# Performance work log

Measured on AMD Instinct MI355X. Metric: run time of the kernel, lower is better.

## Reference

```python
import jax, jax.numpy as jnp
import numpy as np

DIM = 512
NUM_HEADS = 4
SCALE = 1.0 / np.sqrt(DIM)  # note: module scales by 1/sqrt(dim), not 1/sqrt(head_dim)


def setup_inputs() -> dict:
    key = jax.random.key(0)
    k1, k2, k3, k4, k5, k6 = jax.random.split(key, 6)
    B, N, M, C = 8, 2048, 2048, DIM
    bound = 1.0 / np.sqrt(C)
    return {
        "F1": jax.random.normal(k1, (B, N, C), dtype=jnp.float32),
        "F2": jax.random.normal(k2, (B, M, C), dtype=jnp.float32),
        "W_qkv": jax.random.uniform(k3, (C, C), jnp.float32, -bound, bound),
        "b_qkv": jax.random.uniform(k4, (C,), jnp.float32, -bound, bound),
        "W_proj": jax.random.uniform(k5, (C, C), jnp.float32, -bound, bound),
        "b_proj": jax.random.uniform(k6, (C,), jnp.float32, -bound, bound),
    }


def reference(F1, F2, W_qkv, b_qkv, W_proj, b_proj):
    B, N, C = F1.shape
    M = F2.shape[1]
    H, D = NUM_HEADS, C // NUM_HEADS
    # shared qkv projection (same weights for q, k and v in the original module)
    q = (F1 @ W_qkv + b_qkv).reshape(B, N, H, D)  # queries from F1
    kv = (F2 @ W_qkv + b_qkv).reshape(B, M, H, D)  # keys == values from F2
    attn = jnp.einsum("bnhd,bmhd->bhnm", q * SCALE, kv)
    attn = jax.nn.softmax(attn, axis=-1)
    x = jnp.einsum("bhnm,bmhd->bnhd", attn, kv).reshape(B, N, C)
    return x @ W_proj + b_proj
```

## Files before the change

kernel.cpp:

```cpp
#include <hip/hip_runtime.h>
#include <math.h>


typedef __attribute__((ext_vector_type(8))) short s16x8;
typedef __attribute__((ext_vector_type(4))) float f32x4;

#define C_DIM 512
#define HDIM  128
#define NROWS 16384
#define SCALE_Q 0.04419417382415922f
#define LOG2E   1.4426950408889634f

__device__ __forceinline__ unsigned short f2bf(float f) {
    union { float f; unsigned u; } v; v.f = f;
    unsigned r = v.u + 0x7fffu + ((v.u >> 16) & 1u);
    return (unsigned short)(r >> 16);
}

__device__ __forceinline__ void async16(const void* g, void* l) {
    __builtin_amdgcn_global_load_lds(
        (const __attribute__((address_space(1))) void*)g,
        (__attribute__((address_space(3))) void*)l, 16, 0, 0);
}

__global__ __launch_bounds__(256)
void conv_bf16_2(const float* __restrict__ s0, const float* __restrict__ s1,
                 unsigned short* __restrict__ d0, unsigned short* __restrict__ d1,
                 int n8) {
    const float* src = blockIdx.y ? s1 : s0;
    unsigned short* dst = blockIdx.y ? d1 : d0;
    int i = blockIdx.x * 256 + threadIdx.x;
    if (i >= n8) return;
    float4 a = ((const float4*)src)[2 * i];
    float4 b = ((const float4*)src)[2 * i + 1];
    union { unsigned short us[8]; uint4 v; } o;
    o.us[0] = f2bf(a.x); o.us[1] = f2bf(a.y); o.us[2] = f2bf(a.z); o.us[3] = f2bf(a.w);
    o.us[4] = f2bf(b.x); o.us[5] = f2bf(b.y); o.us[6] = f2bf(b.z); o.us[7] = f2bf(b.w);
    ((uint4*)dst)[i] = o.v;
}

__global__ __launch_bounds__(256)
void wconv_t2(const float* __restrict__ W0, const float* __restrict__ W1,
              unsigned short* __restrict__ T0, unsigned short* __restrict__ T1) {
    const float* W = blockIdx.z ? W1 : W0;
    unsigned short* Wt = blockIdx.z ? T1 : T0;
    __shared__ float t[64][65];
    const int k0 = blockIdx.y * 64, n0 = blockIdx.x * 64;
    const int c = threadIdx.x & 63, r0 = threadIdx.x >> 6;
#pragma unroll
    for (int r = r0; r < 64; r += 4)
        t[r][c] = W[(size_t)(k0 + r) * C_DIM + n0 + c];
    __syncthreads();
#pragma unroll
    for (int r = r0; r < 64; r += 4)
        Wt[(size_t)(n0 + r) * C_DIM + k0 + c] = f2bf(t[c][r]);
}

__global__ __launch_bounds__(256)
void kv_transpose(const unsigned short* __restrict__ KV,
                  unsigned short* __restrict__ KVT) {
    __shared__ unsigned short t[64][66];
    const int key0 = blockIdx.x * 64;
    const int d0   = blockIdx.y * 64;
    const int bh   = blockIdx.z;
    const int b    = bh >> 2, h = bh & 3;
    const int c = threadIdx.x & 63, r0 = threadIdx.x >> 6;
    const unsigned short* src = KV + ((size_t)(b * 2048 + key0)) * C_DIM + h * HDIM + d0;
#pragma unroll
    for (int r = r0; r < 64; r += 4)
        t[r][c] = src[(size_t)r * C_DIM + c];
    __syncthreads();
    unsigned short* dst = KVT + ((size_t)(bh * HDIM + d0)) * 2048 + key0;
#pragma unroll
    for (int r = r0; r < 64; r += 4)
        dst[(size_t)r * 2048 + c] = t[c][r];
}

template <int OUT_BF16>
__global__ __launch_bounds__(256, 3)
void gemm_bt(const unsigned short* __restrict__ A,
             const unsigned short* __restrict__ Bt,
             const float* __restrict__ bias,
             void* __restrict__ Cv, float oscTop, int topRows) {
    __shared__ __align__(16) unsigned short As[128][64];
    __shared__ __align__(16) unsigned short Bs[128][64];

    const int tid  = threadIdx.x;
    const int wid  = tid >> 6;
    const int lane = tid & 63;
    const int lr   = lane & 15;
    const int quad = lane >> 4;
    const int wm   = wid >> 1;
    const int wn   = wid & 1;
    const int rowBase = blockIdx.y * 128;
    const int colBase = blockIdx.x * 128;
    const int srow = lane >> 3;
    const int soff = srow * C_DIM + (((lane & 7) ^ (srow & 7)) * 8);
    const float osc = (rowBase < topRows) ? oscTop : 1.0f;

    f32x4 acc[4][4];
#pragma unroll
    for (int i = 0; i < 4; i++)
#pragma unroll
        for (int j = 0; j < 4; j++) acc[i][j] = (f32x4)0.0f;

    for (int kt = 0; kt < 8; kt++) {
        const int k0 = kt * 64;
        __syncthreads();
#pragma unroll
        for (int i = 0; i < 4; i++) {
            const int R = wid * 32 + i * 8;
            async16(A  + (size_t)(rowBase + R) * C_DIM + k0 + soff, &As[R][0]);
            async16(Bt + (size_t)(colBase + R) * C_DIM + k0 + soff, &Bs[R][0]);
        }
        __syncthreads();

#pragma unroll
        for (int s = 0; s < 2; s++) {
            s16x8 af[4], bf[4];
#pragma unroll
            for (int i = 0; i < 4; i++)
                af[i] = *(const s16x8*)&As[wm * 64 + i * 16 + lr][((s * 4 + quad) ^ (lr & 7)) * 8];
#pragma unroll
            for (int j = 0; j < 4; j++)
                bf[j] = *(const s16x8*)&Bs[wn * 64 + j * 16 + lr][((s * 4 + quad) ^ (lr & 7)) * 8];
#pragma unroll
            for (int i = 0; i < 4; i++)
#pragma unroll
                for (int j = 0; j < 4; j++)
                    acc[i][j] = __builtin_amdgcn_mfma_f32_16x16x32_bf16(af[i], bf[j], acc[i][j], 0, 0, 0);
        }
    }

    float bcol[4];
#pragma unroll
    for (int j = 0; j < 4; j++)
        bcol[j] = bias[colBase + wn * 64 + j * 16 + lr];
#pragma unroll
    for (int i = 0; i < 4; i++) {
#pragma unroll
        for (int j = 0; j < 4; j++) {
            const int col = colBase + wn * 64 + j * 16 + lr;
#pragma unroll
            for (int r = 0; r < 4; r++) {
                const int row = rowBase + wm * 64 + i * 16 + quad * 4 + r;
                float v = (acc[i][j][r] + bcol[j]) * osc;
                if (OUT_BF16)
                    ((unsigned short*)Cv)[(size_t)row * C_DIM + col] = f2bf(v);
                else
                    ((float*)Cv)[(size_t)row * C_DIM + col] = v;
            }
        }
    }
}

__global__ __launch_bounds__(256, 2)
void cross_attn(const unsigned short* __restrict__ Q,
                const unsigned short* __restrict__ KV,
                const unsigned short* __restrict__ KVT,
                unsigned short* __restrict__ X) {
    __shared__ __align__(16) unsigned short Kt[2][64][128];
    __shared__ __align__(16) unsigned short Vt[2][128][64];
    __shared__ __align__(16) unsigned short Pl[4][32][64];

    const int tid  = threadIdx.x;
    const int wid  = tid >> 6;
    const int lane = tid & 63;
    const int lr   = lane & 15;
    const int quad = lane >> 4;

    const int wg   = blockIdx.x;
    const int xcd  = wg & 7;
    const int slot = wg >> 3;
    const int p    = xcd + 8 * (slot & 3);
    const int xblk = slot >> 2;
    const int b    = p >> 2;
    const int h    = p & 3;
    const int hoff = h * HDIM;
    const size_t qrow0  = (size_t)b * 2048 + xblk * 128 + wid * 32;
    const size_t kvrow0 = (size_t)b * 2048;

    s16x8 qf[2][4];
#pragma unroll
    for (int i = 0; i < 2; i++)
#pragma unroll
        for (int kk = 0; kk < 4; kk++)
            qf[i][kk] = *(const s16x8*)(Q + (qrow0 + i * 16 + lr) * C_DIM + hoff + kk * 32 + quad * 8);

    const unsigned short* pK[4];
    const unsigned short* pV[4];
#pragma unroll
    for (int a = 0; a < 4; a++) {
        const int rk  = a * 4 + (lane >> 4);
        const int pp  = lane & 15;
        const int ck  = (pp & 8) | ((pp ^ (rk & 7)) & 7);
        const int key = 4 * rk + wid;
        pK[a] = KV + (kvrow0 + key) * C_DIM + hoff + ck * 8;
        const int d  = wid * 32 + a * 8 + (lane >> 3);
        const int cv = (lane & 7) ^ (lane >> 3);
        pV[a] = KVT + ((size_t)((b * 4 + h) * HDIM + d)) * 2048 + cv * 8;
    }

    f32x4 O[2][8];
#pragma unroll
    for (int i = 0; i < 2; i++)
#pragma unroll
        for (int dt = 0; dt < 8; dt++) O[i][dt] = (f32x4)0.0f;
    float lacc[2][4];
#pragma unroll
    for (int i = 0; i < 2; i++)
#pragma unroll
        for (int r = 0; r < 4; r++) lacc[i][r] = 0.0f;

#pragma unroll
    for (int a = 0; a < 4; a++) {
        async16(pK[a], &Kt[0][wid * 16 + a * 4][0]);
        async16(pV[a], &Vt[0][wid * 32 + a * 8][0]);
    }

    for (int kt = 0; kt < 32; kt++) {
        const int cur = kt & 1;
        if (kt < 31) {
            const size_t key0 = (size_t)(kt + 1) * 64;
#pragma unroll
            for (int a = 0; a < 4; a++) {
                async16(pK[a] + key0 * C_DIM, &Kt[cur ^ 1][wid * 16 + a * 4][0]);
                async16(pV[a] + key0,         &Vt[cur ^ 1][wid * 32 + a * 8][0]);
            }
            asm volatile("s_waitcnt vmcnt(8)" ::: "memory");
        } else {
            asm volatile("s_waitcnt vmcnt(0)" ::: "memory");
        }
        __builtin_amdgcn_sched_barrier(0);
        __builtin_amdgcn_s_barrier();
        __builtin_amdgcn_sched_barrier(0);

        f32x4 s[2][4];
#pragma unroll
        for (int i = 0; i < 2; i++)
#pragma unroll
            for (int j = 0; j < 4; j++) s[i][j] = (f32x4)0.0f;
#pragma unroll
        for (int kk = 0; kk < 4; kk++) {
#pragma unroll
            for (int j = 0; j < 4; j++) {
                s16x8 kf = *(const s16x8*)&Kt[cur][j * 16 + lr][((kk * 4 + quad) ^ (lr & 7)) * 8];
                s[0][j] = __builtin_amdgcn_mfma_f32_16x16x32_bf16(qf[0][kk], kf, s[0][j], 0, 0, 0);
                s[1][j] = __builtin_amdgcn_mfma_f32_16x16x32_bf16(qf[1][kk], kf, s[1][j], 0, 0, 0);
            }
        }

#pragma unroll
        for (int i = 0; i < 2; i++) {
#pragma unroll
            for (int r = 0; r < 4; r++) {
                float p0 = exp2f(s[i][0][r]);
                float p1 = exp2f(s[i][1][r]);
                float p2 = exp2f(s[i][2][r]);
                float p3 = exp2f(s[i][3][r]);
                lacc[i][r] += (p0 + p1) + (p2 + p3);
                uint2 pk;
                pk.x = (unsigned)f2bf(p0) | ((unsigned)f2bf(p1) << 16);
                pk.y = (unsigned)f2bf(p2) | ((unsigned)f2bf(p3) << 16);
                const int row = i * 16 + quad * 4 + r;
                *(uint2*)&Pl[wid][row][(((lr >> 1) ^ (row & 7)) * 8) + (lr & 1) * 4] = pk;
            }
        }

#pragma unroll
        for (int kk = 0; kk < 2; kk++) {
            s16x8 pa0 = *(const s16x8*)&Pl[wid][lr][((kk * 4 + quad) ^ (lr & 7)) * 8];
            s16x8 pa1 = *(const s16x8*)&Pl[wid][16 + lr][((kk * 4 + quad) ^ (lr & 7)) * 8];
#pragma unroll
            for (int dt = 0; dt < 8; dt++) {
                s16x8 vf = *(const s16x8*)&Vt[cur][dt * 16 + lr][((kk * 4 + quad) ^ (lr & 7)) * 8];
                O[0][dt] = __builtin_amdgcn_mfma_f32_16x16x32_bf16(pa0, vf, O[0][dt], 0, 0, 0);
                O[1][dt] = __builtin_amdgcn_mfma_f32_16x16x32_bf16(pa1, vf, O[1][dt], 0, 0, 0);
            }
        }

        asm volatile("s_waitcnt lgkmcnt(0)" ::: "memory");
        __builtin_amdgcn_sched_barrier(0);
        __builtin_amdgcn_s_barrier();
        __builtin_amdgcn_sched_barrier(0);
    }

#pragma unroll
    for (int i = 0; i < 2; i++) {
#pragma unroll
        for (int r = 0; r < 4; r++) {
            float l = lacc[i][r];
#pragma unroll
            for (int off = 1; off < 16; off <<= 1)
                l += __shfl_xor(l, off);
            const float inv = 1.0f / l;
            const size_t row = (qrow0 + i * 16 + quad * 4 + r) * C_DIM + hoff;
#pragma unroll
            for (int dt = 0; dt < 8; dt++)
                X[row + dt * 16 + lr] = f2bf(O[i][dt][r] * inv);
        }
    }
}

extern "C" void kernel_launch(void* const* d_in, const int* in_sizes, int n_in,
                              void* d_out, int out_size, void* d_ws, size_t ws_size,
                              hipStream_t stream) {
    const float* F1     = (const float*)d_in[0];
    const float* F2     = (const float*)d_in[1];
    const float* W_qkv  = (const float*)d_in[2];
    const float* b_qkv  = (const float*)d_in[3];
    const float* W_proj = (const float*)d_in[4];
    const float* b_proj = (const float*)d_in[5];
    float* out = (float*)d_out;

    const size_t NC = (size_t)NROWS * C_DIM;
    unsigned short* F1b = (unsigned short*)d_ws;
    unsigned short* F2b = F1b + NC;
    unsigned short* Qw  = F2b + NC;
    unsigned short* KVw = Qw  + NC;
    unsigned short* Wqt = KVw + NC;
    unsigned short* Wpt = Wqt + C_DIM * C_DIM;
    unsigned short* Xw  = F1b;
    unsigned short* KVT = F2b;

    dim3 blk(256);

    conv_bf16_2<<<dim3(NC / 8 / 256, 2), blk, 0, stream>>>(F1, F2, F1b, F2b, (int)(NC / 8));
    wconv_t2<<<dim3(8, 8, 2), blk, 0, stream>>>(W_qkv, W_proj, Wqt, Wpt);

    gemm_bt<1><<<dim3(4, 256), blk, 0, stream>>>(F1b, Wqt, b_qkv, Qw, SCALE_Q * LOG2E, NROWS);
    kv_transpose<<<dim3(32, 2, 32), blk, 0, stream>>>(KVw, KVT);
    cross_attn<<<dim3(512), blk, 0, stream>>>(Qw, KVw, KVT, Xw);
    gemm_bt<0><<<dim3(4, 128), blk, 0, stream>>>(Xw, Wpt, b_proj, out, 1.0f, 0);
}
```

Baseline: 262.0 us.

## Split attention block across 8 waves of 16 query rows each

The attention kernel now launches 512 threads per block, with each of 8 waves owning 16 query rows instead of 4 waves owning 32. K/V tile loads are spread over twice as many threads, and the per-wave register footprint (accumulators, Q fragments, scores) is halved, targeting higher occupancy and more latency hiding. exp2f is replaced by the raw hardware exp2 builtin. The trade-off is that each K/V fragment read from LDS now feeds only one MFMA instead of two, which doubles LDS read traffic per unit of compute.

Result: faster. 250.7 us (-4.3%).

```diff
diff --git a/kernel.cpp b/kernel.cpp
--- a/kernel.cpp
+++ b/kernel.cpp
@@ -154,14 +154,14 @@
     }
 }
 
-__global__ __launch_bounds__(256, 2)
+__global__ __launch_bounds__(512, 4)
 void cross_attn(const unsigned short* __restrict__ Q,
                 const unsigned short* __restrict__ KV,
                 const unsigned short* __restrict__ KVT,
                 unsigned short* __restrict__ X) {
     __shared__ __align__(16) unsigned short Kt[2][64][128];
     __shared__ __align__(16) unsigned short Vt[2][128][64];
-    __shared__ __align__(16) unsigned short Pl[4][32][64];
+    __shared__ __align__(16) unsigned short Pl[8][16][64];
 
     const int tid  = threadIdx.x;
     const int wid  = tid >> 6;
@@ -177,45 +177,39 @@
     const int b    = p >> 2;
     const int h    = p & 3;
     const int hoff = h * HDIM;
-    const size_t qrow0  = (size_t)b * 2048 + xblk * 128 + wid * 32;
+    const size_t qrow0  = (size_t)b * 2048 + xblk * 128 + wid * 16;
     const size_t kvrow0 = (size_t)b * 2048;
 
-    s16x8 qf[2][4];
-#pragma unroll
-    for (int i = 0; i < 2; i++)
-#pragma unroll
-        for (int kk = 0; kk < 4; kk++)
-            qf[i][kk] = *(const s16x8*)(Q + (qrow0 + i * 16 + lr) * C_DIM + hoff + kk * 32 + quad * 8);
-
-    const unsigned short* pK[4];
-    const unsigned short* pV[4];
-#pragma unroll
-    for (int a = 0; a < 4; a++) {
-        const int rk  = a * 4 + (lane >> 4);
+    s16x8 qf[4];
+#pragma unroll
+    for (int kk = 0; kk < 4; kk++)
+        qf[kk] = *(const s16x8*)(Q + (qrow0 + lr) * C_DIM + hoff + kk * 32 + quad * 8);
+
+    const unsigned short* pK[2];
+    const unsigned short* pV[2];
+#pragma unroll
+    for (int a = 0; a < 2; a++) {
+        const int R   = wid * 8 + a * 4 + (lane >> 4);
         const int pp  = lane & 15;
-        const int ck  = (pp & 8) | ((pp ^ (rk & 7)) & 7);
-        const int key = 4 * rk + wid;
+        const int ck  = (pp & 8) | ((pp ^ (R & 7)) & 7);
+        const int key = 4 * (R & 15) + (R >> 4);
         pK[a] = KV + (kvrow0 + key) * C_DIM + hoff + ck * 8;
-        const int d  = wid * 32 + a * 8 + (lane >> 3);
+        const int d  = wid * 16 + a * 8 + (lane >> 3);
         const int cv = (lane & 7) ^ (lane >> 3);
         pV[a] = KVT + ((size_t)((b * 4 + h) * HDIM + d)) * 2048 + cv * 8;
     }
 
-    f32x4 O[2][8];
-#pragma unroll
-    for (int i = 0; i < 2; i++)
-#pragma unroll
-        for (int dt = 0; dt < 8; dt++) O[i][dt] = (f32x4)0.0f;
-    float lacc[2][4];
-#pragma unroll
-    for (int i = 0; i < 2; i++)
-#pragma unroll
-        for (int r = 0; r < 4; r++) lacc[i][r] = 0.0f;
-
-#pragma unroll
-    for (int a = 0; a < 4; a++) {
-        async16(pK[a], &Kt[0][wid * 16 + a * 4][0]);
-        async16(pV[a], &Vt[0][wid * 32 + a * 8][0]);
+    f32x4 O[8];
+#pragma unroll
+    for (int dt = 0; dt < 8; dt++) O[dt] = (f32x4)0.0f;
+    float lacc[4];
+#pragma unroll
+    for (int r = 0; r < 4; r++) lacc[r] = 0.0f;
+
+#pragma unroll
+    for (int a = 0; a < 2; a++) {
+        async16(pK[a], &Kt[0][wid * 8 + a * 4][0]);
+        async16(pV[a], &Vt[0][wid * 16 + a * 8][0]);
     }
 
     for (int kt = 0; kt < 32; kt++) {
@@ -223,11 +217,11 @@
         if (kt < 31) {
             const size_t key0 = (size_t)(kt + 1) * 64;
 #pragma unroll
-            for (int a = 0; a < 4; a++) {
-                async16(pK[a] + key0 * C_DIM, &Kt[cur ^ 1][wid * 16 + a * 4][0]);
-                async16(pV[a] + key0,         &Vt[cur ^ 1][wid * 32 + a * 8][0]);
+            for (int a = 0; a < 2; a++) {
+                async16(pK[a] + key0 * C_DIM, &Kt[cur ^ 1][wid * 8 + a * 4][0]);
+                async16(pV[a] + key0,         &Vt[cur ^ 1][wid * 16 + a * 8][0]);
             }
-            asm volatile("s_waitcnt vmcnt(8)" ::: "memory");
+            asm volatile("s_waitcnt vmcnt(4)" ::: "memory");
         } else {
             asm volatile("s_waitcnt vmcnt(0)" ::: "memory");
         }
@@ -235,47 +229,39 @@
         __builtin_amdgcn_s_barrier();
         __builtin_amdgcn_sched_barrier(0);
 
-        f32x4 s[2][4];
-#pragma unroll
-        for (int i = 0; i < 2; i++)
-#pragma unroll
-            for (int j = 0; j < 4; j++) s[i][j] = (f32x4)0.0f;
+        f32x4 s[4];
+#pragma unroll
+        for (int j = 0; j < 4; j++) s[j] = (f32x4)0.0f;
 #pragma unroll
         for (int kk = 0; kk < 4; kk++) {
 #pragma unroll
             for (int j = 0; j < 4; j++) {
                 s16x8 kf = *(const s16x8*)&Kt[cur][j * 16 + lr][((kk * 4 + quad) ^ (lr & 7)) * 8];
-                s[0][j] = __builtin_amdgcn_mfma_f32_16x16x32_bf16(qf[0][kk], kf, s[0][j], 0, 0, 0);
-                s[1][j] = __builtin_amdgcn_mfma_f32_16x16x32_bf16(qf[1][kk], kf, s[1][j], 0, 0, 0);
+                s[j] = __builtin_amdgcn_mfma_f32_16x16x32_bf16(qf[kk], kf, s[j], 0, 0, 0);
             }
         }
 
 #pragma unroll
-        for (int i = 0; i < 2; i++) {
-#pragma unroll
-            for (int r = 0; r < 4; r++) {
-                float p0 = exp2f(s[i][0][r]);
-                float p1 = exp2f(s[i][1][r]);
-                float p2 = exp2f(s[i][2][r]);
-                float p3 = exp2f(s[i][3][r]);
-                lacc[i][r] += (p0 + p1) + (p2 + p3);
-                uint2 pk;
-                pk.x = (unsigned)f2bf(p0) | ((unsigned)f2bf(p1) << 16);
-                pk.y = (unsigned)f2bf(p2) | ((unsigned)f2bf(p3) << 16);
-                const int row = i * 16 + quad * 4 + r;
-                *(uint2*)&Pl[wid][row][(((lr >> 1) ^ (row & 7)) * 8) + (lr & 1) * 4] = pk;
-            }
+        for (int r = 0; r < 4; r++) {
+            float p0 = __builtin_amdgcn_exp2f(s[0][r]);
+            float p1 = __builtin_amdgcn_exp2f(s[1][r]);
+            float p2 = __builtin_amdgcn_exp2f(s[2][r]);
+            float p3 = __builtin_amdgcn_exp2f(s[3][r]);
+            lacc[r] += (p0 + p1) + (p2 + p3);
+            uint2 pk;
+            pk.x = (unsigned)f2bf(p0) | ((unsigned)f2bf(p1) << 16);
+            pk.y = (unsigned)f2bf(p2) | ((unsigned)f2bf(p3) << 16);
+            const int row = quad * 4 + r;
+            *(uint2*)&Pl[wid][row][(((lr >> 1) ^ (row & 7)) * 8) + (lr & 1) * 4] = pk;
         }
 
 #pragma unroll
         for (int kk = 0; kk < 2; kk++) {
-            s16x8 pa0 = *(const s16x8*)&Pl[wid][lr][((kk * 4 + quad) ^ (lr & 7)) * 8];
-            s16x8 pa1 = *(const s16x8*)&Pl[wid][16 + lr][((kk * 4 + quad) ^ (lr & 7)) * 8];
+            s16x8 pa = *(const s16x8*)&Pl[wid][lr][((kk * 4 + quad) ^ (lr & 7)) * 8];
 #pragma unroll
             for (int dt = 0; dt < 8; dt++) {
                 s16x8 vf = *(const s16x8*)&Vt[cur][dt * 16 + lr][((kk * 4 + quad) ^ (lr & 7)) * 8];
-                O[0][dt] = __builtin_amdgcn_mfma_f32_16x16x32_bf16(pa0, vf, O[0][dt], 0, 0, 0);
-                O[1][dt] = __builtin_amdgcn_mfma_f32_16x16x32_bf16(pa1, vf, O[1][dt], 0, 0, 0);
+                O[dt] = __builtin_amdgcn_mfma_f32_16x16x32_bf16(pa, vf, O[dt], 0, 0, 0);
             }
         }
 
@@ -286,19 +272,16 @@
     }
 
 #pragma unroll
-    for (int i = 0; i < 2; i++) {
-#pragma unroll
-        for (int r = 0; r < 4; r++) {
-            float l = lacc[i][r];
-#pragma unroll
-            for (int off = 1; off < 16; off <<= 1)
-                l += __shfl_xor(l, off);
-            const float inv = 1.0f / l;
-            const size_t row = (qrow0 + i * 16 + quad * 4 + r) * C_DIM + hoff;
-#pragma unroll
-            for (int dt = 0; dt < 8; dt++)
-                X[row + dt * 16 + lr] = f2bf(O[i][dt][r] * inv);
-        }
+    for (int r = 0; r < 4; r++) {
+        float l = lacc[r];
+#pragma unroll
+        for (int off = 1; off < 16; off <<= 1)
+            l += __shfl_xor(l, off);
+        const float inv = 1.0f / l;
+        const size_t row = (qrow0 + quad * 4 + r) * C_DIM + hoff;
+#pragma unroll
+        for (int dt = 0; dt < 8; dt++)
+            X[row + dt * 16 + lr] = f2bf(O[dt][r] * inv);
     }
 }
 
@@ -330,6 +313,6 @@
 
     gemm_bt<1><<<dim3(4, 256), blk, 0, stream>>>(F1b, Wqt, b_qkv, Qw, SCALE_Q * LOG2E, NROWS);
     kv_transpose<<<dim3(32, 2, 32), blk, 0, stream>>>(KVw, KVT);
-    cross_attn<<<dim3(512), blk, 0, stream>>>(Qw, KVw, KVT, Xw);
+    cross_attn<<<dim3(512), dim3(512), 0, stream>>>(Qw, KVw, KVT, Xw);
     gemm_bt<0><<<dim3(4, 128), blk, 0, stream>>>(Xw, Wpt, b_proj, out, 1.0f, 0);
 }
```

## Widen attention blocks to 8 waves with triple-buffered K/V prefetch

Applied to the files above, without the earlier changes.

The attention kernel now runs 512-thread blocks covering 256 query rows, so each K/V tile loaded into LDS is shared by twice as many waves and each wave issues half as many async loads. The K/V staging goes from double to triple buffering with a prefetch distance of two tiles, and the waitcnt logic is adjusted for the last iterations. exp2f is replaced with the hardware exp2 intrinsic. The cost is more LDS per block (about 112 KB) and half as many blocks in the grid, which may reduce occupancy or load balance across CUs.

After: 252.5 us. -3.6%, faster.

```diff
diff --git a/kernel.cpp b/kernel.cpp
--- a/kernel.cpp
+++ b/kernel.cpp
@@ -154,14 +154,14 @@
     }
 }
 
-__global__ __launch_bounds__(256, 2)
+__global__ __launch_bounds__(512, 2)
 void cross_attn(const unsigned short* __restrict__ Q,
                 const unsigned short* __restrict__ KV,
                 const unsigned short* __restrict__ KVT,
                 unsigned short* __restrict__ X) {
-    __shared__ __align__(16) unsigned short Kt[2][64][128];
-    __shared__ __align__(16) unsigned short Vt[2][128][64];
-    __shared__ __align__(16) unsigned short Pl[4][32][64];
+    __shared__ __align__(16) unsigned short Kt[3][64][128];
+    __shared__ __align__(16) unsigned short Vt[3][128][64];
+    __shared__ __align__(16) unsigned short Pl[8][32][64];
 
     const int tid  = threadIdx.x;
     const int wid  = tid >> 6;
@@ -177,7 +177,7 @@
     const int b    = p >> 2;
     const int h    = p & 3;
     const int hoff = h * HDIM;
-    const size_t qrow0  = (size_t)b * 2048 + xblk * 128 + wid * 32;
+    const size_t qrow0  = (size_t)b * 2048 + xblk * 256 + wid * 32;
     const size_t kvrow0 = (size_t)b * 2048;
 
     s16x8 qf[2][4];
@@ -187,16 +187,16 @@
         for (int kk = 0; kk < 4; kk++)
             qf[i][kk] = *(const s16x8*)(Q + (qrow0 + i * 16 + lr) * C_DIM + hoff + kk * 32 + quad * 8);
 
-    const unsigned short* pK[4];
-    const unsigned short* pV[4];
-#pragma unroll
-    for (int a = 0; a < 4; a++) {
-        const int rk  = a * 4 + (lane >> 4);
+    const unsigned short* pK[2];
+    const unsigned short* pV[2];
+#pragma unroll
+    for (int a = 0; a < 2; a++) {
+        const int R   = wid * 8 + a * 4 + (lane >> 4);
         const int pp  = lane & 15;
-        const int ck  = (pp & 8) | ((pp ^ (rk & 7)) & 7);
-        const int key = 4 * rk + wid;
+        const int ck  = (pp & 8) | ((pp ^ (R & 7)) & 7);
+        const int key = 4 * (R & 15) + (R >> 4);
         pK[a] = KV + (kvrow0 + key) * C_DIM + hoff + ck * 8;
-        const int d  = wid * 32 + a * 8 + (lane >> 3);
+        const int d  = wid * 16 + a * 8 + (lane >> 3);
         const int cv = (lane & 7) ^ (lane >> 3);
         pV[a] = KVT + ((size_t)((b * 4 + h) * HDIM + d)) * 2048 + cv * 8;
     }
@@ -213,21 +213,28 @@
         for (int r = 0; r < 4; r++) lacc[i][r] = 0.0f;
 
 #pragma unroll
-    for (int a = 0; a < 4; a++) {
-        async16(pK[a], &Kt[0][wid * 16 + a * 4][0]);
-        async16(pV[a], &Vt[0][wid * 32 + a * 8][0]);
-    }
-
+    for (int t = 0; t < 2; t++) {
+        const size_t key0 = (size_t)t * 64;
+#pragma unroll
+        for (int a = 0; a < 2; a++) {
+            async16(pK[a] + key0 * C_DIM, &Kt[t][wid * 8 + a * 4][0]);
+            async16(pV[a] + key0,         &Vt[t][wid * 16 + a * 8][0]);
+        }
+    }
+
+    int cur = 0;
     for (int kt = 0; kt < 32; kt++) {
-        const int cur = kt & 1;
-        if (kt < 31) {
-            const size_t key0 = (size_t)(kt + 1) * 64;
-#pragma unroll
-            for (int a = 0; a < 4; a++) {
-                async16(pK[a] + key0 * C_DIM, &Kt[cur ^ 1][wid * 16 + a * 4][0]);
-                async16(pV[a] + key0,         &Vt[cur ^ 1][wid * 32 + a * 8][0]);
+        if (kt < 30) {
+            const int nbuf = (cur + 2 >= 3) ? cur - 1 : cur + 2;
+            const size_t key0 = (size_t)(kt + 2) * 64;
+#pragma unroll
+            for (int a = 0; a < 2; a++) {
+                async16(pK[a] + key0 * C_DIM, &Kt[nbuf][wid * 8 + a * 4][0]);
+                async16(pV[a] + key0,         &Vt[nbuf][wid * 16 + a * 8][0]);
             }
             asm volatile("s_waitcnt vmcnt(8)" ::: "memory");
+        } else if (kt == 30) {
+            asm volatile("s_waitcnt vmcnt(4)" ::: "memory");
         } else {
             asm volatile("s_waitcnt vmcnt(0)" ::: "memory");
         }
@@ -254,10 +261,10 @@
         for (int i = 0; i < 2; i++) {
 #pragma unroll
             for (int r = 0; r < 4; r++) {
-                float p0 = exp2f(s[i][0][r]);
-                float p1 = exp2f(s[i][1][r]);
-                float p2 = exp2f(s[i][2][r]);
-                float p3 = exp2f(s[i][3][r]);
+                float p0 = __builtin_amdgcn_exp2f(s[i][0][r]);
+                float p1 = __builtin_amdgcn_exp2f(s[i][1][r]);
+                float p2 = __builtin_amdgcn_exp2f(s[i][2][r]);
+                float p3 = __builtin_amdgcn_exp2f(s[i][3][r]);
                 lacc[i][r] += (p0 + p1) + (p2 + p3);
                 uint2 pk;
                 pk.x = (unsigned)f2bf(p0) | ((unsigned)f2bf(p1) << 16);
@@ -283,6 +290,8 @@
         __builtin_amdgcn_sched_barrier(0);
         __builtin_amdgcn_s_barrier();
         __builtin_amdgcn_sched_barrier(0);
+
+        cur = (cur + 1 >= 3) ? 0 : cur + 1;
     }
 
 #pragma unroll
@@ -330,6 +339,6 @@
 
     gemm_bt<1><<<dim3(4, 256), blk, 0, stream>>>(F1b, Wqt, b_qkv, Qw, SCALE_Q * LOG2E, NROWS);
     kv_transpose<<<dim3(32, 2, 32), blk, 0, stream>>>(KVw, KVT);
-    cross_attn<<<dim3(512), blk, 0, stream>>>(Qw, KVw, KVT, Xw);
+    cross_attn<<<dim3(256), dim3(512), 0, stream>>>(Qw, KVw, KVT, Xw);
     gemm_bt<0><<<dim3(4, 128), blk, 0, stream>>>(Xw, Wpt, b_proj, out, 1.0f, 0);
 }
```

## Compute transposed scores so P stays in registers as MFMA A-operand

Applied to the files above, without the earlier changes.

Swaps the QK^T MFMA operand order so each lane holds score values in the layout that the PV MFMA needs as its A operand. The K tile load order is permuted so that the key ordering lines up, which lets the P tile skip its round-trip through LDS along with the extra LDS writes and reads that came with it. Row-sum accumulation becomes per-lane with cross-quad shuffles, and exp2 uses the hardware builtin. This relies on the key permutation matching the V layout exactly, since any mismatch gives wrong sums.

Result: faster. 240.2 us (-8.3%).

```diff
diff --git a/kernel.cpp b/kernel.cpp
--- a/kernel.cpp
+++ b/kernel.cpp
@@ -161,7 +161,6 @@
                 unsigned short* __restrict__ X) {
     __shared__ __align__(16) unsigned short Kt[2][64][128];
     __shared__ __align__(16) unsigned short Vt[2][128][64];
-    __shared__ __align__(16) unsigned short Pl[4][32][64];
 
     const int tid  = threadIdx.x;
     const int wid  = tid >> 6;
@@ -191,10 +190,10 @@
     const unsigned short* pV[4];
 #pragma unroll
     for (int a = 0; a < 4; a++) {
-        const int rk  = a * 4 + (lane >> 4);
+        const int R   = wid * 16 + a * 4 + (lane >> 4);
+        const int key = 32 * (R >> 5) + 8 * ((R >> 2) & 3) + 4 * ((R >> 4) & 1) + (R & 3);
         const int pp  = lane & 15;
-        const int ck  = (pp & 8) | ((pp ^ (rk & 7)) & 7);
-        const int key = 4 * rk + wid;
+        const int ck  = (pp & 8) | ((pp ^ (R & 7)) & 7);
         pK[a] = KV + (kvrow0 + key) * C_DIM + hoff + ck * 8;
         const int d  = wid * 32 + a * 8 + (lane >> 3);
         const int cv = (lane & 7) ^ (lane >> 3);
@@ -206,11 +205,8 @@
     for (int i = 0; i < 2; i++)
 #pragma unroll
         for (int dt = 0; dt < 8; dt++) O[i][dt] = (f32x4)0.0f;
-    float lacc[2][4];
-#pragma unroll
-    for (int i = 0; i < 2; i++)
-#pragma unroll
-        for (int r = 0; r < 4; r++) lacc[i][r] = 0.0f;
+    float lacc[2];
+    lacc[0] = 0.0f; lacc[1] = 0.0f;
 
 #pragma unroll
     for (int a = 0; a < 4; a++) {
@@ -245,37 +241,41 @@
 #pragma unroll
             for (int j = 0; j < 4; j++) {
                 s16x8 kf = *(const s16x8*)&Kt[cur][j * 16 + lr][((kk * 4 + quad) ^ (lr & 7)) * 8];
-                s[0][j] = __builtin_amdgcn_mfma_f32_16x16x32_bf16(qf[0][kk], kf, s[0][j], 0, 0, 0);
-                s[1][j] = __builtin_amdgcn_mfma_f32_16x16x32_bf16(qf[1][kk], kf, s[1][j], 0, 0, 0);
-            }
-        }
-
+                s[0][j] = __builtin_amdgcn_mfma_f32_16x16x32_bf16(kf, qf[0][kk], s[0][j], 0, 0, 0);
+                s[1][j] = __builtin_amdgcn_mfma_f32_16x16x32_bf16(kf, qf[1][kk], s[1][j], 0, 0, 0);
+            }
+        }
+
+        s16x8 pa[2][2];
 #pragma unroll
         for (int i = 0; i < 2; i++) {
 #pragma unroll
-            for (int r = 0; r < 4; r++) {
-                float p0 = exp2f(s[i][0][r]);
-                float p1 = exp2f(s[i][1][r]);
-                float p2 = exp2f(s[i][2][r]);
-                float p3 = exp2f(s[i][3][r]);
-                lacc[i][r] += (p0 + p1) + (p2 + p3);
-                uint2 pk;
-                pk.x = (unsigned)f2bf(p0) | ((unsigned)f2bf(p1) << 16);
-                pk.y = (unsigned)f2bf(p2) | ((unsigned)f2bf(p3) << 16);
-                const int row = i * 16 + quad * 4 + r;
-                *(uint2*)&Pl[wid][row][(((lr >> 1) ^ (row & 7)) * 8) + (lr & 1) * 4] = pk;
+            for (int kk = 0; kk < 2; kk++) {
+                float p0 = __builtin_amdgcn_exp2f(s[i][2 * kk][0]);
+                float p1 = __builtin_amdgcn_exp2f(s[i][2 * kk][1]);
+                float p2 = __builtin_amdgcn_exp2f(s[i][2 * kk][2]);
+                float p3 = __builtin_amdgcn_exp2f(s[i][2 * kk][3]);
+                float p4 = __builtin_amdgcn_exp2f(s[i][2 * kk + 1][0]);
+                float p5 = __builtin_amdgcn_exp2f(s[i][2 * kk + 1][1]);
+                float p6 = __builtin_amdgcn_exp2f(s[i][2 * kk + 1][2]);
+                float p7 = __builtin_amdgcn_exp2f(s[i][2 * kk + 1][3]);
+                lacc[i] += ((p0 + p1) + (p2 + p3)) + ((p4 + p5) + (p6 + p7));
+                union { unsigned short us[8]; s16x8 v; } pu;
+                pu.us[0] = f2bf(p0); pu.us[1] = f2bf(p1);
+                pu.us[2] = f2bf(p2); pu.us[3] = f2bf(p3);
+                pu.us[4] = f2bf(p4); pu.us[5] = f2bf(p5);
+                pu.us[6] = f2bf(p6); pu.us[7] = f2bf(p7);
+                pa[i][kk] = pu.v;
             }
         }
 
 #pragma unroll
         for (int kk = 0; kk < 2; kk++) {
-            s16x8 pa0 = *(const s16x8*)&Pl[wid][lr][((kk * 4 + quad) ^ (lr & 7)) * 8];
-            s16x8 pa1 = *(const s16x8*)&Pl[wid][16 + lr][((kk * 4 + quad) ^ (lr & 7)) * 8];
 #pragma unroll
             for (int dt = 0; dt < 8; dt++) {
                 s16x8 vf = *(const s16x8*)&Vt[cur][dt * 16 + lr][((kk * 4 + quad) ^ (lr & 7)) * 8];
-                O[0][dt] = __builtin_amdgcn_mfma_f32_16x16x32_bf16(pa0, vf, O[0][dt], 0, 0, 0);
-                O[1][dt] = __builtin_amdgcn_mfma_f32_16x16x32_bf16(pa1, vf, O[1][dt], 0, 0, 0);
+                O[0][dt] = __builtin_amdgcn_mfma_f32_16x16x32_bf16(pa[0][kk], vf, O[0][dt], 0, 0, 0);
+                O[1][dt] = __builtin_amdgcn_mfma_f32_16x16x32_bf16(pa[1][kk], vf, O[1][dt], 0, 0, 0);
             }
         }
 
@@ -287,13 +287,12 @@
 
 #pragma unroll
     for (int i = 0; i < 2; i++) {
+        float l = lacc[i];
+        l += __shfl_xor(l, 16);
+        l += __shfl_xor(l, 32);
 #pragma unroll
         for (int r = 0; r < 4; r++) {
-            float l = lacc[i][r];
-#pragma unroll
-            for (int off = 1; off < 16; off <<= 1)
-                l += __shfl_xor(l, off);
-            const float inv = 1.0f / l;
+            const float inv = 1.0f / __shfl(l, quad * 4 + r);
             const size_t row = (qrow0 + i * 16 + quad * 4 + r) * C_DIM + hoff;
 #pragma unroll
             for (int dt = 0; dt < 8; dt++)
```
